# Kernel tuning notes

Hardware: AMD Instinct MI355X
Metric: run time of the kernel (lower is better)

Reference implementation:

```python
import jax, jax.numpy as jnp
import numpy as np

HID = 2880; H = 64; HKV = 8; D = 64; G = H // HKV
WIN = 128; BLK = 128
BASE = 150000.0; FACTOR = 32.0; ORIG = 4096.0; BETA_FAST = 32.0; BETA_SLOW = 1.0


def _yarn_cos_sin(pos):
    # vLLM YaRN (neox style): blend interpolated/extrapolated inv_freq + mscale
    half = D // 2
    pf = BASE ** (np.arange(0, D, 2, dtype=np.float64) / D)
    extrap = 1.0 / pf
    interp = 1.0 / (FACTOR * pf)
    def cdim(num_rot):
        return D * np.log(ORIG / (num_rot * 2 * np.pi)) / (2 * np.log(BASE))
    low = max(np.floor(cdim(BETA_FAST)), 0.0)
    high = min(np.ceil(cdim(BETA_SLOW)), D - 1.0)
    ramp = np.clip((np.arange(half, dtype=np.float64) - low) / max(high - low, 1e-3), 0.0, 1.0)
    ext_mask = 1.0 - ramp  # 1 -> extrapolate (high freq), 0 -> interpolate
    inv_freq = jnp.asarray(interp * (1.0 - ext_mask) + extrap * ext_mask, jnp.float32)
    mscale = np.float32(0.1 * np.log(FACTOR) + 1.0)
    freqs = pos.astype(jnp.float32)[:, None] * inv_freq[None, :]  # [S, D/2]
    return jnp.cos(freqs) * mscale, jnp.sin(freqs) * mscale


def _rope(x, cos, sin):
    # neox-style rotate-halves; x: [S, h, D], cos/sin: [S, D/2]
    x1, x2 = x[..., : D // 2], x[..., D // 2 :]
    c, s = cos[:, None, :], sin[:, None, :]
    return jnp.concatenate([x1 * c - x2 * s, x2 * c + x1 * s], axis=-1)


def reference(hidden_states, position_ids, w_qkv, b_qkv, w_o, b_o, sinks):
    S = hidden_states.shape[0]
    qkv = hidden_states @ w_qkv + b_qkv  # [S, (H+2*HKV)*D]
    q = qkv[:, : H * D].reshape(S, H, D)
    k = qkv[:, H * D : H * D + HKV * D].reshape(S, HKV, D)
    v = qkv[:, H * D + HKV * D :].reshape(S, HKV, D)
    cos, sin = _yarn_cos_sin(position_ids)
    q = _rope(q, cos, sin) * (D ** -0.5)
    k = _rope(k, cos, sin)

    # Blocked sliding-window causal attention (window = 128 tokens incl. self).
    nb = S // BLK
    qb = q.reshape(nb, BLK, HKV, G, D)
    kb = k.reshape(nb, BLK, HKV, D)
    vb = v.reshape(nb, BLK, HKV, D)
    kk = jnp.concatenate([jnp.concatenate([jnp.zeros_like(kb[:1]), kb[:-1]], 0), kb], 1)  # [nb, 2B, HKV, D]
    vv = jnp.concatenate([jnp.concatenate([jnp.zeros_like(vb[:1]), vb[:-1]], 0), vb], 1)

    scores = jnp.einsum('nqkgd,nmkd->nkgqm', qb, kk)  # [nb, HKV, G, B, 2B]
    a = jnp.arange(BLK)[:, None]
    m = jnp.arange(2 * BLK)[None, :]
    delta = a + BLK - m  # query_pos - key_pos
    band = (delta >= 0) & (delta < WIN)
    kpos_ok = ((jnp.arange(nb)[:, None, None] - 1) * BLK + m) >= 0
    valid = (band[None] & kpos_ok)[:, None, None]  # [nb,1,1,B,2B]
    scores = jnp.where(valid, scores, jnp.float32(-1e30))

    # Per-head learnable sink logit participates in softmax but has no value.
    sink = sinks.reshape(HKV, G)[None, :, :, None]  # [1,HKV,G,1]
    mx = jnp.maximum(jnp.max(scores, -1), sink)  # [nb,HKV,G,B]
    p = jnp.exp(scores - mx[..., None])
    denom = p.sum(-1) + jnp.exp(sink - mx)
    out = jnp.einsum('nkgqm,nmkd->nqkgd', p, vv) / denom.transpose(0, 3, 1, 2)[..., None]
    attn = out.reshape(S, H * D)
    return attn @ w_o + b_o


def setup_inputs() -> dict:
    key = jax.random.key(0)
    ks = jax.random.split(key, 6)
    S = 4096
    return {
        'hidden_states': jax.random.normal(ks[0], (S, HID), jnp.float32),
        'position_ids': jnp.arange(S),
        'w_qkv': jax.random.normal(ks[1], (HID, (H + 2 * HKV) * D), jnp.float32) * 0.02,
        'b_qkv': jax.random.normal(ks[2], ((H + 2 * HKV) * D,), jnp.float32) * 0.02,
        'w_o': jax.random.normal(ks[3], (H * D, HID), jnp.float32) * 0.02,
        'b_o': jax.random.normal(ks[4], (HID,), jnp.float32) * 0.02,
        'sinks': jax.random.normal(ks[5], (H,), jnp.float32),
    }
```

## Files before the change

### kernel.cpp

```cpp
#include <hip/hip_runtime.h>

#define DEV __device__ __forceinline__

typedef unsigned short u16;
typedef unsigned int   u32;
typedef __attribute__((ext_vector_type(8))) short short8;
typedef __attribute__((ext_vector_type(4))) float f32x4;

DEV u16 f2bf(float f) {
  u32 u = __builtin_bit_cast(u32, f);
  u = (u + 0x7FFFu + ((u >> 16) & 1u)) >> 16;
  return (u16)u;
}

DEV void gl_lds16(const void* g, void* l) {
  __builtin_amdgcn_global_load_lds((const __attribute__((address_space(1))) void*)g,
                                   (__attribute__((address_space(3))) void*)l, 16, 0, 0);
}

DEV f32x4 mfma_bf16(short8 a, short8 b, f32x4 c) {
  return __builtin_amdgcn_mfma_f32_16x16x32_bf16(a, b, c, 0, 0, 0);
}

__global__ __launch_bounds__(256) void f32_to_bf16_k(const float* __restrict__ in,
                                                     u16* __restrict__ out, int n4) {
  int stride = gridDim.x * 256;
  for (int i = blockIdx.x * 256 + threadIdx.x; i < n4; i += stride) {
    float4 v = ((const float4*)in)[i];
    u32 lo = (u32)f2bf(v.x) | ((u32)f2bf(v.y) << 16);
    u32 hi = (u32)f2bf(v.z) | ((u32)f2bf(v.w) << 16);
    ((uint2*)out)[i] = make_uint2(lo, hi);
  }
}

__global__ __launch_bounds__(256) void transpose_to_bf16_k(const float* __restrict__ W,
                                                           u16* __restrict__ WT,
                                                           int K, int N) {
  __shared__ u16 T[64][72];
  int k0 = blockIdx.x * 64, n0 = blockIdx.y * 64;
  int t = threadIdx.x;
#pragma unroll
  for (int i = 0; i < 4; ++i) {
    int c = t + i * 256;
    int kr = c >> 4, nc = (c & 15) * 4;
    float4 v = make_float4(0.f, 0.f, 0.f, 0.f);
    if (n0 + nc < N) v = *(const float4*)(W + (size_t)(k0 + kr) * N + n0 + nc);
    T[nc + 0][kr] = f2bf(v.x);
    T[nc + 1][kr] = f2bf(v.y);
    T[nc + 2][kr] = f2bf(v.z);
    T[nc + 3][kr] = f2bf(v.w);
  }
  __syncthreads();
#pragma unroll
  for (int i = 0; i < 2; ++i) {
    int c = t + i * 256;
    int nr = c >> 3, kc = (c & 7) * 8;
    int4 v = *(const int4*)&T[nr][kc];
    *(int4*)(WT + (size_t)(n0 + nr) * K + k0 + kc) = v;
  }
}

__global__ __launch_bounds__(256) void gemm_bt_k(const u16* __restrict__ A,
                                                 const u16* __restrict__ BT,
                                                 float* __restrict__ C,
                                                 const float* __restrict__ bias,
                                                 int K, int ldc, int Nguard, int Ntiles) {
  __shared__ u16 As[128 * 32];
  __shared__ u16 Bs[128 * 32];
  int bid = blockIdx.x;
  int m0 = (bid / Ntiles) * 128, n0 = (bid % Ntiles) * 128;
  int t = threadIdx.x, w = t >> 6, l = t & 63;
  int lr = l & 15, lg = l >> 4;
  int wr = w >> 1, wc = w & 1;

  const u16* Ag0 = A  + (size_t)(m0 + (t >> 2)) * K + (t & 3) * 8;
  const u16* Ag1 = Ag0 + (size_t)64 * K;
  const u16* Bg0 = BT + (size_t)(n0 + (t >> 2)) * K + (t & 3) * 8;
  const u16* Bg1 = Bg0 + (size_t)64 * K;
  u16* AsW0 = As + w * 512;  u16* AsW1 = As + 2048 + w * 512;
  u16* BsW0 = Bs + w * 512;  u16* BsW1 = Bs + 2048 + w * 512;

  f32x4 acc[4][4];
#pragma unroll
  for (int i = 0; i < 4; ++i)
#pragma unroll
    for (int j = 0; j < 4; ++j) acc[i][j] = (f32x4){0.f, 0.f, 0.f, 0.f};

  for (int kt = 0; kt < K; kt += 32) {
    gl_lds16(Ag0 + kt, AsW0);
    gl_lds16(Ag1 + kt, AsW1);
    gl_lds16(Bg0 + kt, BsW0);
    gl_lds16(Bg1 + kt, BsW1);
    __syncthreads();
    short8 af[4], bfr[4];
#pragma unroll
    for (int i = 0; i < 4; ++i) af[i]  = *(const short8*)(As + (wr * 64 + i * 16 + lr) * 32 + lg * 8);
#pragma unroll
    for (int j = 0; j < 4; ++j) bfr[j] = *(const short8*)(Bs + (wc * 64 + j * 16 + lr) * 32 + lg * 8);
#pragma unroll
    for (int i = 0; i < 4; ++i)
#pragma unroll
      for (int j = 0; j < 4; ++j)
        acc[i][j] = mfma_bf16(af[i], bfr[j], acc[i][j]);
    __syncthreads();
  }

#pragma unroll
  for (int j = 0; j < 4; ++j) {
    int col = n0 + wc * 64 + j * 16 + lr;
    if (col < Nguard) {
      float bv = bias[col];
#pragma unroll
      for (int i = 0; i < 4; ++i) {
        size_t base = (size_t)(m0 + wr * 64 + i * 16 + lg * 4) * ldc + col;
#pragma unroll
        for (int r = 0; r < 4; ++r)
          C[base + (size_t)r * ldc] = acc[i][j][r] + bv;
      }
    }
  }
}

__global__ __launch_bounds__(256) void rope_k(const float* __restrict__ qkv,
                                              const int* __restrict__ pos_ids,
                                              u16* __restrict__ qb, u16* __restrict__ kb,
                                              u16* __restrict__ vb) {
  int s = blockIdx.x;
  int t = threadIdx.x;
  __shared__ float cs[32], sn[32];
  if (t < 32) {
    int i = t;
    const double PI = 3.14159265358979323846;
    double pf = exp(log(150000.0) * ((double)i / 32.0));
    double extrap = 1.0 / pf;
    double interp = extrap / 32.0;
    double l2b = 2.0 * log(150000.0);
    double low  = floor(64.0 * log(4096.0 / (32.0 * 2.0 * PI)) / l2b);
    double high = ceil (64.0 * log(4096.0 / ( 1.0 * 2.0 * PI)) / l2b);
    if (low < 0.0) low = 0.0;
    if (high > 63.0) high = 63.0;
    double ramp = ((double)i - low) / fmax(high - low, 0.001);
    ramp = fmin(fmax(ramp, 0.0), 1.0);
    float invf = (float)(interp * ramp + extrap * (1.0 - ramp));
    float fr = (float)pos_ids[s] * invf;
    float mscale = (float)(0.1 * log(32.0) + 1.0);
    cs[i] = cosf(fr) * mscale;
    sn[i] = sinf(fr) * mscale;
  }
  __syncthreads();
  const float* row = qkv + (size_t)s * 5120;
#pragma unroll
  for (int j = 0; j < 8; ++j) {
    int p = t + j * 256;
    int hh = p >> 5, i = p & 31;
    float x1 = row[hh * 64 + i], x2 = row[hh * 64 + i + 32];
    float c = cs[i], sv = sn[i];
    qb[(size_t)s * 4096 + hh * 64 + i]      = f2bf((x1 * c - x2 * sv) * 0.125f);
    qb[(size_t)s * 4096 + hh * 64 + i + 32] = f2bf((x2 * c + x1 * sv) * 0.125f);
  }
  {
    int kvh = t >> 5, i = t & 31;
    float x1 = row[4096 + kvh * 64 + i], x2 = row[4096 + kvh * 64 + i + 32];
    float c = cs[i], sv = sn[i];
    kb[(size_t)s * 512 + kvh * 64 + i]      = f2bf(x1 * c - x2 * sv);
    kb[(size_t)s * 512 + kvh * 64 + i + 32] = f2bf(x2 * c + x1 * sv);
  }
  vb[(size_t)s * 512 + t * 2]     = f2bf(row[4608 + t * 2]);
  vb[(size_t)s * 512 + t * 2 + 1] = f2bf(row[4608 + t * 2 + 1]);
}

__global__ __launch_bounds__(256, 1) void attn_k(const u16* __restrict__ qb,
                                                 const u16* __restrict__ kb,
                                                 const u16* __restrict__ vb,
                                                 const float* __restrict__ sinks,
                                                 u16* __restrict__ attnb) {
  int n = blockIdx.x, h = blockIdx.y;
  int kvh = h >> 3;
  int t = threadIdx.x, w = t >> 6, l = t & 63;
  int lr = l & 15, lg = l >> 4;
  __shared__ u16 Ks[256 * 72];
  __shared__ u16 VT[64 * 264];
  __shared__ u16 Ps[4][32 * 136];
  float sink = sinks[h];

  for (int c = t; c < 2048; c += 256) {
    int m = c >> 3, j = c & 7;
    int s = n * 128 - 128 + m;
    int4 kvl = make_int4(0, 0, 0, 0), vvl = make_int4(0, 0, 0, 0);
    if (s >= 0) {
      kvl = *(const int4*)(kb + (size_t)s * 512 + kvh * 64 + j * 8);
      vvl = *(const int4*)(vb + (size_t)s * 512 + kvh * 64 + j * 8);
    }
    *(int4*)(Ks + m * 72 + j * 8) = kvl;
    const u16* ve = (const u16*)&vvl;
#pragma unroll
    for (int e = 0; e < 8; ++e) VT[(j * 8 + e) * 264 + m] = ve[e];
  }
  __syncthreads();

  short8 aq[2][2];
#pragma unroll
  for (int i = 0; i < 2; ++i)
#pragma unroll
    for (int kk = 0; kk < 2; ++kk)
      aq[i][kk] = *(const short8*)(qb + (size_t)(n * 128 + w * 32 + i * 16 + lr) * 4096
                                      + h * 64 + kk * 32 + lg * 8);

  f32x4 p[2][16];
#pragma unroll
  for (int ct = 0; ct < 16; ++ct) {
    short8 b0 = *(const short8*)(Ks + (ct * 16 + lr) * 72 + lg * 8);
    short8 b1 = *(const short8*)(Ks + (ct * 16 + lr) * 72 + 32 + lg * 8);
#pragma unroll
    for (int i = 0; i < 2; ++i) {
      f32x4 z = (f32x4){0.f, 0.f, 0.f, 0.f};
      z = mfma_bf16(aq[i][0], b0, z);
      z = mfma_bf16(aq[i][1], b1, z);
      p[i][ct] = z;
    }
  }

  float invden[2][4];
#pragma unroll
  for (int i = 0; i < 2; ++i) {
#pragma unroll
    for (int r = 0; r < 4; ++r) {
      int q = w * 32 + i * 16 + lg * 4 + r;
      float best = -1e30f;
#pragma unroll
      for (int ct = 0; ct < 16; ++ct) {
        int m = ct * 16 + lr;
        int delta = q + 128 - m;
        bool valid = (delta >= 0) & (delta < 128) & ((n > 0) | (m >= 128));
        float v = valid ? p[i][ct][r] : -1e30f;
        p[i][ct][r] = v;
        best = fmaxf(best, v);
      }
#pragma unroll
      for (int d = 1; d < 16; d <<= 1) best = fmaxf(best, __shfl_xor(best, d, 64));
      best = fmaxf(best, sink);
      float sum = 0.f;
#pragma unroll
      for (int ct = 0; ct < 16; ++ct) {
        float e = expf(p[i][ct][r] - best);
        p[i][ct][r] = e;
        sum += e;
      }
#pragma unroll
      for (int d = 1; d < 16; d <<= 1) sum += __shfl_xor(sum, d, 64);
      sum += expf(sink - best);
      invden[i][r] = 1.0f / sum;
    }
  }

  f32x4 o[2][4];
#pragma unroll
  for (int qt = 0; qt < 2; ++qt)
#pragma unroll
    for (int dt = 0; dt < 4; ++dt) o[qt][dt] = (f32x4){0.f, 0.f, 0.f, 0.f};

  u16* Pw = Ps[w];
#pragma unroll
  for (int half = 0; half < 2; ++half) {
#pragma unroll
    for (int i = 0; i < 2; ++i)
#pragma unroll
      for (int ct = 0; ct < 8; ++ct)
#pragma unroll
        for (int r = 0; r < 4; ++r)
          Pw[(i * 16 + lg * 4 + r) * 136 + ct * 16 + lr] = f2bf(p[i][half * 8 + ct][r]);
#pragma unroll
    for (int ks = 0; ks < 4; ++ks) {
      short8 bv[4];
#pragma unroll
      for (int dt = 0; dt < 4; ++dt)
        bv[dt] = *(const short8*)(VT + (dt * 16 + lr) * 264 + half * 128 + ks * 32 + lg * 8);
#pragma unroll
      for (int qt = 0; qt < 2; ++qt) {
        short8 av = *(const short8*)(Pw + (qt * 16 + lr) * 136 + ks * 32 + lg * 8);
#pragma unroll
        for (int dt = 0; dt < 4; ++dt)
          o[qt][dt] = mfma_bf16(av, bv[dt], o[qt][dt]);
      }
    }
  }

#pragma unroll
  for (int qt = 0; qt < 2; ++qt)
#pragma unroll
    for (int dt = 0; dt < 4; ++dt)
#pragma unroll
      for (int r = 0; r < 4; ++r) {
        int row = n * 128 + w * 32 + qt * 16 + lg * 4 + r;
        int col = h * 64 + dt * 16 + lr;
        attnb[(size_t)row * 4096 + col] = f2bf(o[qt][dt][r] * invden[qt][r]);
      }
}

extern "C" void kernel_launch(void* const* d_in, const int* in_sizes, int n_in,
                              void* d_out, int out_size, void* d_ws, size_t ws_size,
                              hipStream_t stream) {
  const float* hidden = (const float*)d_in[0];
  const int*   pos    = (const int*)d_in[1];
  const float* w_qkv  = (const float*)d_in[2];
  const float* b_qkv  = (const float*)d_in[3];
  const float* w_o    = (const float*)d_in[4];
  const float* b_o    = (const float*)d_in[5];
  const float* sinks  = (const float*)d_in[6];
  float* out = (float*)d_out;
  char* ws = (char*)d_ws;

  u16*  hbf   = (u16*)(ws + 0);
  u16*  wqkvT = (u16*)(ws + 23592960);
  u16*  attnb = (u16*)(ws + 0);
  float* qkv  = (float*)(ws + 53084160);
  u16*  q_bf  = (u16*)(ws + 136970240);
  u16*  k_bf  = (u16*)(ws + 170524672);
  u16*  v_bf  = (u16*)(ws + 174718976);
  u16*  woT   = (u16*)(ws + 178913280);

  f32_to_bf16_k<<<2048, 256, 0, stream>>>(hidden, hbf, 4096 * 2880 / 4);
  transpose_to_bf16_k<<<dim3(2880 / 64, 5120 / 64), 256, 0, stream>>>(w_qkv, wqkvT, 2880, 5120);
  transpose_to_bf16_k<<<dim3(4096 / 64, 2944 / 64), 256, 0, stream>>>(w_o, woT, 4096, 2880);
  gemm_bt_k<<<32 * 40, 256, 0, stream>>>(hbf, wqkvT, qkv, b_qkv, 2880, 5120, 5120, 40);
  rope_k<<<4096, 256, 0, stream>>>(qkv, pos, q_bf, k_bf, v_bf);
  attn_k<<<dim3(32, 64), 256, 0, stream>>>(q_bf, k_bf, v_bf, sinks, attnb);
  gemm_bt_k<<<32 * 23, 256, 0, stream>>>(attnb, woT, out, b_o, 4096, 2880, 2880, 23);

  (void)in_sizes; (void)n_in; (void)out_size; (void)ws_size;
}
```

Before: 628.0 us.

## Replace GEMM with 256x256 8-wave pipelined kernel and fuse RoPE epilogue

```diff
diff --git a/kernel.cpp b/kernel.cpp
--- a/kernel.cpp
+++ b/kernel.cpp
@@ -21,6 +21,9 @@
 DEV f32x4 mfma_bf16(short8 a, short8 b, f32x4 c) {
   return __builtin_amdgcn_mfma_f32_16x16x32_bf16(a, b, c, 0, 0, 0);
 }
+
+#define BAR() do { asm volatile("" ::: "memory"); __builtin_amdgcn_s_barrier(); asm volatile("" ::: "memory"); } while (0)
+#define WAITV(N) asm volatile("s_waitcnt vmcnt(" #N ")" ::: "memory")
 
 __global__ __launch_bounds__(256) void f32_to_bf16_k(const float* __restrict__ in,
                                                      u16* __restrict__ out, int n4) {
@@ -60,113 +63,199 @@
   }
 }
 
-__global__ __launch_bounds__(256) void gemm_bt_k(const u16* __restrict__ A,
-                                                 const u16* __restrict__ BT,
-                                                 float* __restrict__ C,
-                                                 const float* __restrict__ bias,
-                                                 int K, int ldc, int Nguard, int Ntiles) {
-  __shared__ u16 As[128 * 32];
-  __shared__ u16 Bs[128 * 32];
+template<int MH>
+DEV void rd_a(short8 (&af)[4][2], const u16* lb, int rowA, int sl0, int sl1) {
+#pragma unroll
+  for (int ii = 0; ii < 4; ++ii) {
+    af[ii][0] = *(const short8*)(lb + rowA + (MH * 64 + ii * 16) * 64 + sl0);
+    af[ii][1] = *(const short8*)(lb + rowA + (MH * 64 + ii * 16) * 64 + sl1);
+  }
+}
+template<int JJ>
+DEV void rd_b(short8 (&bf)[4][2], const u16* lb, int rowB, int sl0, int sl1) {
+  bf[JJ][0] = *(const short8*)(lb + rowB + JJ * 16 * 64 + sl0);
+  bf[JJ][1] = *(const short8*)(lb + rowB + JJ * 16 * 64 + sl1);
+}
+template<int MH, int J0, int J1>
+DEV void phase_mfma(f32x4 (&acc)[8][4], short8 (&af)[4][2], short8 (&bf)[4][2]) {
+  __builtin_amdgcn_s_setprio(1);
+#pragma unroll
+  for (int ii = 0; ii < 4; ++ii) {
+    acc[MH * 4 + ii][J0] = mfma_bf16(af[ii][0], bf[J0][0], acc[MH * 4 + ii][J0]);
+    acc[MH * 4 + ii][J0] = mfma_bf16(af[ii][1], bf[J0][1], acc[MH * 4 + ii][J0]);
+    acc[MH * 4 + ii][J1] = mfma_bf16(af[ii][0], bf[J1][0], acc[MH * 4 + ii][J1]);
+    acc[MH * 4 + ii][J1] = mfma_bf16(af[ii][1], bf[J1][1], acc[MH * 4 + ii][J1]);
+  }
+  __builtin_amdgcn_s_setprio(0);
+}
+DEV void stage_half(const u16* g0, size_t Ks, u16* l0) {
+  gl_lds16(g0, l0);
+  gl_lds16(g0 + 64 * Ks, l0 + 4096);
+}
+
+template<int MODE>
+__global__ __launch_bounds__(512, 2) void gemm8p_k(
+    const u16* __restrict__ A, const u16* __restrict__ BT,
+    float* __restrict__ C, const float* __restrict__ bias,
+    int K, int Ntiles, int ldc, int Nguard,
+    const int* __restrict__ posids,
+    u16* __restrict__ qout, u16* __restrict__ kout, u16* __restrict__ vout) {
+  __shared__ u16 lds[65536];
+  const int NT = K >> 6;
+  int nwg = gridDim.x;
   int bid = blockIdx.x;
-  int m0 = (bid / Ntiles) * 128, n0 = (bid % Ntiles) * 128;
+  int swz = (bid & 7) * (nwg >> 3) + (bid >> 3);
+  int m0 = (swz / Ntiles) * 256, n0 = (swz % Ntiles) * 256;
+
   int t = threadIdx.x, w = t >> 6, l = t & 63;
   int lr = l & 15, lg = l >> 4;
-  int wr = w >> 1, wc = w & 1;
-
-  const u16* Ag0 = A  + (size_t)(m0 + (t >> 2)) * K + (t & 3) * 8;
-  const u16* Ag1 = Ag0 + (size_t)64 * K;
-  const u16* Bg0 = BT + (size_t)(n0 + (t >> 2)) * K + (t & 3) * 8;
-  const u16* Bg1 = Bg0 + (size_t)64 * K;
-  u16* AsW0 = As + w * 512;  u16* AsW1 = As + 2048 + w * 512;
-  u16* BsW0 = Bs + w * 512;  u16* BsW1 = Bs + 2048 + w * 512;
-
-  f32x4 acc[4][4];
-#pragma unroll
-  for (int i = 0; i < 4; ++i)
+  int wm = w >> 2, wn = w & 3;
+  int rl = t >> 3;
+  int ss = (t & 7) ^ (rl & 7);
+  const u16* Asrc = A + (size_t)(m0 + rl) * K + ss * 8;
+  const u16* Bsrc = BT + (size_t)(n0 + rl) * K + ss * 8;
+  int wofs = w * 512;
+  int rowA = (wm * 128 + lr) * 64;
+  int rowB = (wn * 64 + lr) * 64;
+  int sl0 = ((lg) ^ (lr & 7)) * 8;
+  int sl1 = ((4 + lg) ^ (lr & 7)) * 8;
+
+  f32x4 acc[8][4];
+#pragma unroll
+  for (int i = 0; i < 8; ++i)
 #pragma unroll
     for (int j = 0; j < 4; ++j) acc[i][j] = (f32x4){0.f, 0.f, 0.f, 0.f};
 
-  for (int kt = 0; kt < K; kt += 32) {
-    gl_lds16(Ag0 + kt, AsW0);
-    gl_lds16(Ag1 + kt, AsW1);
-    gl_lds16(Bg0 + kt, BsW0);
-    gl_lds16(Bg1 + kt, BsW1);
-    __syncthreads();
-    short8 af[4], bfr[4];
-#pragma unroll
-    for (int i = 0; i < 4; ++i) af[i]  = *(const short8*)(As + (wr * 64 + i * 16 + lr) * 32 + lg * 8);
-#pragma unroll
-    for (int j = 0; j < 4; ++j) bfr[j] = *(const short8*)(Bs + (wc * 64 + j * 16 + lr) * 32 + lg * 8);
-#pragma unroll
-    for (int i = 0; i < 4; ++i)
-#pragma unroll
-      for (int j = 0; j < 4; ++j)
-        acc[i][j] = mfma_bf16(af[i], bfr[j], acc[i][j]);
-    __syncthreads();
-  }
-
-#pragma unroll
-  for (int j = 0; j < 4; ++j) {
-    int col = n0 + wc * 64 + j * 16 + lr;
-    if (col < Nguard) {
-      float bv = bias[col];
-#pragma unroll
-      for (int i = 0; i < 4; ++i) {
-        size_t base = (size_t)(m0 + wr * 64 + i * 16 + lg * 4) * ldc + col;
-#pragma unroll
-        for (int r = 0; r < 4; ++r)
-          C[base + (size_t)r * ldc] = acc[i][j][r] + bv;
-      }
-    }
-  }
-}
-
-__global__ __launch_bounds__(256) void rope_k(const float* __restrict__ qkv,
-                                              const int* __restrict__ pos_ids,
-                                              u16* __restrict__ qb, u16* __restrict__ kb,
-                                              u16* __restrict__ vb) {
-  int s = blockIdx.x;
-  int t = threadIdx.x;
-  __shared__ float cs[32], sn[32];
-  if (t < 32) {
-    int i = t;
-    const double PI = 3.14159265358979323846;
-    double pf = exp(log(150000.0) * ((double)i / 32.0));
-    double extrap = 1.0 / pf;
-    double interp = extrap / 32.0;
-    double l2b = 2.0 * log(150000.0);
-    double low  = floor(64.0 * log(4096.0 / (32.0 * 2.0 * PI)) / l2b);
-    double high = ceil (64.0 * log(4096.0 / ( 1.0 * 2.0 * PI)) / l2b);
-    if (low < 0.0) low = 0.0;
-    if (high > 63.0) high = 63.0;
-    double ramp = ((double)i - low) / fmax(high - low, 0.001);
-    ramp = fmin(fmax(ramp, 0.0), 1.0);
-    float invf = (float)(interp * ramp + extrap * (1.0 - ramp));
-    float fr = (float)pos_ids[s] * invf;
-    float mscale = (float)(0.1 * log(32.0) + 1.0);
-    cs[i] = cosf(fr) * mscale;
-    sn[i] = sinf(fr) * mscale;
-  }
-  __syncthreads();
-  const float* row = qkv + (size_t)s * 5120;
-#pragma unroll
-  for (int j = 0; j < 8; ++j) {
-    int p = t + j * 256;
-    int hh = p >> 5, i = p & 31;
-    float x1 = row[hh * 64 + i], x2 = row[hh * 64 + i + 32];
-    float c = cs[i], sv = sn[i];
-    qb[(size_t)s * 4096 + hh * 64 + i]      = f2bf((x1 * c - x2 * sv) * 0.125f);
-    qb[(size_t)s * 4096 + hh * 64 + i + 32] = f2bf((x2 * c + x1 * sv) * 0.125f);
-  }
-  {
-    int kvh = t >> 5, i = t & 31;
-    float x1 = row[4096 + kvh * 64 + i], x2 = row[4096 + kvh * 64 + i + 32];
-    float c = cs[i], sv = sn[i];
-    kb[(size_t)s * 512 + kvh * 64 + i]      = f2bf(x1 * c - x2 * sv);
-    kb[(size_t)s * 512 + kvh * 64 + i + 32] = f2bf(x2 * c + x1 * sv);
-  }
-  vb[(size_t)s * 512 + t * 2]     = f2bf(row[4608 + t * 2]);
-  vb[(size_t)s * 512 + t * 2 + 1] = f2bf(row[4608 + t * 2 + 1]);
+  stage_half(Bsrc,            K, lds + 16384 + wofs);
+  stage_half(Bsrc + 128 * K,  K, lds + 16384 + 8192 + wofs);
+  stage_half(Asrc,            K, lds + wofs);
+  stage_half(Asrc + 128 * K,  K, lds + 8192 + wofs);
+  if (NT > 1) {
+    stage_half(Bsrc + 64,           K, lds + 32768 + 16384 + wofs);
+    stage_half(Bsrc + 128 * K + 64, K, lds + 32768 + 16384 + 8192 + wofs);
+    stage_half(Asrc + 64,           K, lds + 32768 + wofs);
+  }
+  WAITV(6);
+  BAR();
+
+  int p = 0;
+  short8 af[4][2], bf[4][2];
+  for (int kt = 0; kt < NT; ++kt) {
+    const u16* lb = lds + p * 32768;
+    u16* lo = lds + (p ^ 1) * 32768;
+    u16* lc = lds + p * 32768;
+    size_t kc1 = (size_t)(kt + 1) * 64, kc2 = (size_t)(kt + 2) * 64;
+    rd_a<0>(af, lb, rowA, sl0, sl1);
+    rd_b<0>(bf, lb + 16384, rowB, sl0, sl1);
+    rd_b<1>(bf, lb + 16384, rowB, sl0, sl1);
+    if (kt + 1 < NT) stage_half(Asrc + 128 * K + kc1, K, lo + 8192 + wofs);
+    BAR();
+    phase_mfma<0, 0, 1>(acc, af, bf);
+    BAR();
+    rd_b<2>(bf, lb + 16384, rowB, sl0, sl1);
+    rd_b<3>(bf, lb + 16384, rowB, sl0, sl1);
+    BAR();
+    phase_mfma<0, 2, 3>(acc, af, bf);
+    BAR();
+    rd_a<1>(af, lb, rowA, sl0, sl1);
+    if (kt + 2 < NT) stage_half(Bsrc + kc2, K, lc + 16384 + wofs);
+    BAR();
+    phase_mfma<1, 2, 3>(acc, af, bf);
+    BAR();
+    if (kt + 2 < NT) {
+      stage_half(Bsrc + 128 * K + kc2, K, lc + 16384 + 8192 + wofs);
+      stage_half(Asrc + kc2,           K, lc + wofs);
+    }
+    BAR();
+    phase_mfma<1, 0, 1>(acc, af, bf);
+    if (kt < NT - 1) {
+      if (kt + 2 < NT) { WAITV(6); } else { WAITV(0); }
+    }
+    BAR();
+    p ^= 1;
+  }
+
+  if constexpr (MODE == 0) {
+#pragma unroll
+    for (int jj = 0; jj < 4; ++jj) {
+      int col = n0 + wn * 64 + jj * 16 + lr;
+      if (col < Nguard) {
+        float bv = bias[col];
+#pragma unroll
+        for (int ii = 0; ii < 8; ++ii) {
+          int row = m0 + wm * 128 + ii * 16 + lg * 4;
+#pragma unroll
+          for (int r = 0; r < 4; ++r)
+            C[(size_t)(row + r) * ldc + col] = acc[ii][jj][r] + bv;
+        }
+      }
+    }
+  } else {
+    int colbase = n0 + wn * 64;
+    bool isQ = colbase < 4096;
+    bool isV = colbase >= 4608;
+    if (isV) {
+#pragma unroll
+      for (int jj = 0; jj < 4; ++jj) {
+        int col = colbase + jj * 16 + lr;
+        float bv = bias[col];
+#pragma unroll
+        for (int ii = 0; ii < 8; ++ii) {
+          int row = m0 + wm * 128 + ii * 16 + lg * 4;
+#pragma unroll
+          for (int r = 0; r < 4; ++r)
+            vout[(size_t)(row + r) * 512 + (col - 4608)] = f2bf(acc[ii][jj][r] + bv);
+        }
+      }
+    } else {
+      float invf[2];
+#pragma unroll
+      for (int pp = 0; pp < 2; ++pp) {
+        int f = pp * 16 + lr;
+        const double PI = 3.14159265358979323846;
+        double pf = exp(log(150000.0) * ((double)f / 32.0));
+        double extrap = 1.0 / pf;
+        double interp = extrap / 32.0;
+        double l2b = 2.0 * log(150000.0);
+        double low  = floor(64.0 * log(4096.0 / (32.0 * 2.0 * PI)) / l2b);
+        double high = ceil (64.0 * log(4096.0 / ( 1.0 * 2.0 * PI)) / l2b);
+        if (low < 0.0) low = 0.0;
+        if (high > 63.0) high = 63.0;
+        double ramp = ((double)f - low) / fmax(high - low, 0.001);
+        ramp = fmin(fmax(ramp, 0.0), 1.0);
+        invf[pp] = (float)(interp * ramp + extrap * (1.0 - ramp));
+      }
+      float mscale = (float)(0.1 * log(32.0) + 1.0);
+      float qsc = isQ ? 0.125f : 1.0f;
+#pragma unroll
+      for (int jj = 0; jj < 2; ++jj) {
+        int col_lo = colbase + jj * 16 + lr;
+        int col_hi = col_lo + 32;
+        float blo = bias[col_lo], bhi = bias[col_hi];
+#pragma unroll
+        for (int ii = 0; ii < 8; ++ii) {
+          int row = m0 + wm * 128 + ii * 16 + lg * 4;
+#pragma unroll
+          for (int r = 0; r < 4; ++r) {
+            int ps = posids[row + r];
+            float fr = (float)ps * invf[jj];
+            float c = cosf(fr) * mscale, s = sinf(fr) * mscale;
+            float x1 = acc[ii][jj][r] + blo;
+            float x2 = acc[ii][jj + 2][r] + bhi;
+            float o1 = (x1 * c - x2 * s) * qsc;
+            float o2 = (x2 * c + x1 * s) * qsc;
+            if (isQ) {
+              qout[(size_t)(row + r) * 4096 + col_lo] = f2bf(o1);
+              qout[(size_t)(row + r) * 4096 + col_hi] = f2bf(o2);
+            } else {
+              kout[(size_t)(row + r) * 512 + (col_lo - 4096)] = f2bf(o1);
+              kout[(size_t)(row + r) * 512 + (col_hi - 4096)] = f2bf(o2);
+            }
+          }
+        }
+      }
+    }
+  }
 }
 
 __global__ __launch_bounds__(256, 1) void attn_k(const u16* __restrict__ qb,
@@ -310,22 +399,22 @@
   float* out = (float*)d_out;
   char* ws = (char*)d_ws;
 
-  u16*  hbf   = (u16*)(ws + 0);
-  u16*  wqkvT = (u16*)(ws + 23592960);
-  u16*  attnb = (u16*)(ws + 0);
-  float* qkv  = (float*)(ws + 53084160);
-  u16*  q_bf  = (u16*)(ws + 136970240);
-  u16*  k_bf  = (u16*)(ws + 170524672);
-  u16*  v_bf  = (u16*)(ws + 174718976);
-  u16*  woT   = (u16*)(ws + 178913280);
+  u16* hbf   = (u16*)(ws + 0);
+  u16* attnb = (u16*)(ws + 0);
+  u16* wqkvT = (u16*)(ws + 33554432);
+  u16* woT   = (u16*)(ws + 63045632);
+  u16* q_bf  = (u16*)(ws + 88211456);
+  u16* k_bf  = (u16*)(ws + 121765888);
+  u16* v_bf  = (u16*)(ws + 125960192);
 
   f32_to_bf16_k<<<2048, 256, 0, stream>>>(hidden, hbf, 4096 * 2880 / 4);
   transpose_to_bf16_k<<<dim3(2880 / 64, 5120 / 64), 256, 0, stream>>>(w_qkv, wqkvT, 2880, 5120);
-  transpose_to_bf16_k<<<dim3(4096 / 64, 2944 / 64), 256, 0, stream>>>(w_o, woT, 4096, 2880);
-  gemm_bt_k<<<32 * 40, 256, 0, stream>>>(hbf, wqkvT, qkv, b_qkv, 2880, 5120, 5120, 40);
-  rope_k<<<4096, 256, 0, stream>>>(qkv, pos, q_bf, k_bf, v_bf);
+  transpose_to_bf16_k<<<dim3(4096 / 64, 3072 / 64), 256, 0, stream>>>(w_o, woT, 4096, 2880);
+  gemm8p_k<1><<<16 * 20, 512, 0, stream>>>(hbf, wqkvT, nullptr, b_qkv,
+                                           2880, 20, 0, 5120, pos, q_bf, k_bf, v_bf);
   attn_k<<<dim3(32, 64), 256, 0, stream>>>(q_bf, k_bf, v_bf, sinks, attnb);
-  gemm_bt_k<<<32 * 23, 256, 0, stream>>>(attnb, woT, out, b_o, 4096, 2880, 2880, 23);
+  gemm8p_k<0><<<16 * 12, 512, 0, stream>>>(attnb, woT, out, b_o,
+                                           4096, 12, 2880, 2880, nullptr, nullptr, nullptr, nullptr);
 
   (void)in_sizes; (void)n_in; (void)out_size; (void)ws_size;
 }
```

Result: slower. 673.0 us (+7.2%).
